# Kernel optimization log

Measured on AMD Instinct MI355X. Metric: run time of the kernel, lower is better.

## Reference

```python
import jax, jax.numpy as jnp
import numpy as np

H = 64          # hidden_size
FF = 36         # MLP hidden
B, W, S = 512, 8, 200


def setup_inputs() -> dict:
    key = jax.random.key(0)
    ks = jax.random.split(key, 8)
    query = jax.random.normal(ks[0], (B, H), dtype=jnp.float32)
    k = jax.random.normal(ks[1], (B, W, S, H), dtype=jnp.float32)
    mask = jax.random.randint(ks[2], (B, W, S, 1), 0, 2).astype(bool)
    # MLP params: Linear(4H -> 36), PReLU(scalar), Linear(36 -> 1)
    lim1 = 1.0 / np.sqrt(4 * H)
    W1 = jax.random.uniform(ks[3], (FF, 4 * H), jnp.float32, -lim1, lim1)
    b1 = jax.random.uniform(ks[4], (FF,), jnp.float32, -lim1, lim1)
    prelu_a = jnp.float32(0.25)
    lim2 = 1.0 / np.sqrt(FF)
    W2 = jax.random.uniform(ks[5], (1, FF), jnp.float32, -lim2, lim2)
    b2 = jax.random.uniform(ks[6], (1,), jnp.float32, -lim2, lim2)
    return {"query": query, "key": k, "W1": W1, "b1": b1,
            "prelu_a": prelu_a, "W2": W2, "b2": b2, "mask": mask}


def reference(query, key, W1, b1, prelu_a, W2, b2, mask):
    # broadcast query to (B, W, S, H)
    q = jnp.broadcast_to(query[:, None, None, :], key.shape)
    feat = jnp.concatenate([q, key, q - key, q * key], axis=-1)  # (B,W,S,4H)
    h = jnp.einsum('bwsf,of->bwso', feat, W1) + b1               # (B,W,S,36)
    h = jnp.where(h >= 0, h, prelu_a * h)                        # PReLU
    score = jnp.einsum('bwso,uo->bwsu', h, W2) + b2              # (B,W,S,1)
    # weighted_att=True: mask with -1e4 then softmax over seq_len
    score = jnp.where(mask, jnp.float32(-10000.0), score)
    score = jax.nn.softmax(score, axis=2)
    out = (key * score).sum(axis=2)                              # (B,W,H)
    return out
```

## Files before the change

### kernel.cpp

```cpp
#include <hip/hip_runtime.h>
#include <hip/hip_bf16.h>
#include <math.h>


#define BB   512
#define WW   8
#define SS   200
#define HH   64
#define FFN  36

typedef __attribute__((ext_vector_type(8))) short short8;
typedef __attribute__((ext_vector_type(4))) float f32x4;

__device__ __forceinline__ unsigned short f2bf(float x) {
    __hip_bfloat16 h = __float2bfloat16(x);
    union { __hip_bfloat16 b; unsigned short u; } c; c.b = h;
    return c.u;
}
__device__ __forceinline__ float bf2f(unsigned short h) {
    union { unsigned u; float f; } v; v.u = ((unsigned)h) << 16;
    return v.f;
}

__global__ __launch_bounds__(256)
void precompute_c(const float* __restrict__ query,
                  const float* __restrict__ W1,
                  const float* __restrict__ b1,
                  unsigned short* __restrict__ c_hi_g,
                  float* __restrict__ A_g)
{
    __shared__ float q_s[HH];
    const int b = blockIdx.x, tid = threadIdx.x;
    if (tid < HH) q_s[tid] = query[b * HH + tid];
    __syncthreads();
    for (int idx = tid; idx < 48 * HH; idx += 256) {
        int o = idx >> 6, h = idx & 63;
        float c = 0.0f;
        if (o < FFN) {
            const float* w = W1 + o * 4 * HH;
            c = w[HH + h] - w[2 * HH + h] + w[3 * HH + h] * q_s[h];
        }
        c_hi_g[(size_t)b * 48 * HH + idx] = f2bf(c);
    }
    if (tid < 48) {
        float a = 0.0f;
        if (tid < FFN) {
            const float* w = W1 + tid * 4 * HH;
            a = b1[tid];
            #pragma unroll 8
            for (int h = 0; h < HH; ++h) a += (w[h] + w[2 * HH + h]) * q_s[h];
        }
        A_g[b * 48 + tid] = a;
    }
}

__device__ __forceinline__ void load_tile(const float* __restrict__ kg,
                                          int st, int n, int q,
                                          float4 (&buf)[2][2])
{
    const int s = st * 16 + n;
    const float* p = kg + (size_t)s * HH + q * 8;
    if (s < SS) {
        buf[0][0] = *(const float4*)(p);
        buf[0][1] = *(const float4*)(p + 4);
        buf[1][0] = *(const float4*)(p + 32);
        buf[1][1] = *(const float4*)(p + 36);
    } else {
        const float4 z = make_float4(0.f, 0.f, 0.f, 0.f);
        buf[0][0] = z; buf[0][1] = z; buf[1][0] = z; buf[1][1] = z;
    }
}

__device__ __forceinline__ void compute_tile(const float4 (&buf)[2][2],
                                             const short8 (&Bf)[3][2],
                                             const float (&Ao)[3],
                                             const float (&w2o)[3],
                                             float pa, int st, int q, int n,
                                             float* __restrict__ scw)
{
    short8 Ah[2], Al[2];
    #pragma unroll
    for (int ks = 0; ks < 2; ++ks) {
        const float vv[8] = {buf[ks][0].x, buf[ks][0].y, buf[ks][0].z, buf[ks][0].w,
                             buf[ks][1].x, buf[ks][1].y, buf[ks][1].z, buf[ks][1].w};
        #pragma unroll
        for (int j = 0; j < 8; ++j) {
            const unsigned short hi = f2bf(vv[j]);
            Ah[ks][j] = (short)hi;
            Al[ks][j] = (short)f2bf(vv[j] - bf2f(hi));
        }
    }
    float contrib[4] = {0.f, 0.f, 0.f, 0.f};
    #pragma unroll
    for (int ot = 0; ot < 3; ++ot) {
        f32x4 acc = {0.f, 0.f, 0.f, 0.f};
        acc = __builtin_amdgcn_mfma_f32_16x16x32_bf16(Ah[0], Bf[ot][0], acc, 0, 0, 0);
        acc = __builtin_amdgcn_mfma_f32_16x16x32_bf16(Al[0], Bf[ot][0], acc, 0, 0, 0);
        acc = __builtin_amdgcn_mfma_f32_16x16x32_bf16(Ah[1], Bf[ot][1], acc, 0, 0, 0);
        acc = __builtin_amdgcn_mfma_f32_16x16x32_bf16(Al[1], Bf[ot][1], acc, 0, 0, 0);
        #pragma unroll
        for (int r = 0; r < 4; ++r) {
            float hv = acc[r] + Ao[ot];
            hv = (hv >= 0.0f) ? hv : pa * hv;
            contrib[r] += w2o[ot] * hv;
        }
    }
    #pragma unroll
    for (int m = 1; m <= 8; m <<= 1)
        #pragma unroll
        for (int r = 0; r < 4; ++r)
            contrib[r] += __shfl_xor(contrib[r], m, 64);
    if (n == 0) {
        #pragma unroll
        for (int r = 0; r < 4; ++r)
            scw[st * 16 + q * 4 + r] = contrib[r];
    }
}

__global__ __launch_bounds__(256, 4)
void twb_wave(const float* __restrict__ key,
              const unsigned short* __restrict__ c_hi_g,
              const float* __restrict__ A_g,
              const float* __restrict__ prelu_a,
              const float* __restrict__ W2,
              const int*   __restrict__ mask,
              float*       __restrict__ out)
{
    __shared__ float sc_s[4][208];

    const int tid  = threadIdx.x;
    const int wid  = tid >> 6, lane = tid & 63;
    const int q    = lane >> 4, n = lane & 15;
    const int bw   = blockIdx.x * 4 + wid;
    const int b    = bw >> 3;
    const float* kg = key + (size_t)bw * (SS * HH);
    float* scw = sc_s[wid];

    const unsigned short* cb = c_hi_g + (size_t)b * 48 * HH;
    short8 Bf[3][2];
    float  Ao[3], w2o[3];
    #pragma unroll
    for (int ot = 0; ot < 3; ++ot) {
        const int o = ot * 16 + n;
        #pragma unroll
        for (int ks = 0; ks < 2; ++ks)
            Bf[ot][ks] = *(const short8*)(cb + (size_t)o * HH + ks * 32 + q * 8);
        Ao[ot]  = A_g[b * 48 + o];
        w2o[ot] = (o < FFN) ? W2[o] : 0.0f;
    }
    const float pa = prelu_a[0];
    const int mv0 = mask[bw * SS + lane];
    const int mv1 = mask[bw * SS + 64 + lane];
    const int mv2 = mask[bw * SS + 128 + lane];
    const int mv3 = (lane < 8) ? mask[bw * SS + 192 + lane] : 1;

    float4 bufA[2][2], bufB[2][2];
    load_tile(kg, 0, n, q, bufA);
    for (int st2 = 0; st2 < 6; ++st2) {
        const int st = st2 * 2;
        load_tile(kg, st + 1, n, q, bufB);
        compute_tile(bufA, Bf, Ao, w2o, pa, st, q, n, scw);
        load_tile(kg, st + 2, n, q, bufA);
        compute_tile(bufB, Bf, Ao, w2o, pa, st + 1, q, n, scw);
    }
    compute_tile(bufA, Bf, Ao, w2o, pa, 12, q, n, scw);

    float sv0 = mv0 ? -10000.0f : scw[lane];
    float sv1 = mv1 ? -10000.0f : scw[64 + lane];
    float sv2 = mv2 ? -10000.0f : scw[128 + lane];
    float sv3 = (lane < 8) ? (mv3 ? -10000.0f : scw[192 + lane]) : -3.0e38f;
    float mx = fmaxf(fmaxf(sv0, sv1), fmaxf(sv2, sv3));
    #pragma unroll
    for (int off = 32; off > 0; off >>= 1)
        mx = fmaxf(mx, __shfl_xor(mx, off, 64));
    const float e0 = __expf(sv0 - mx);
    const float e1 = __expf(sv1 - mx);
    const float e2 = __expf(sv2 - mx);
    const float e3 = (lane < 8) ? __expf(sv3 - mx) : 0.0f;
    float ssum = e0 + e1 + e2 + e3;
    #pragma unroll
    for (int off = 32; off > 0; off >>= 1)
        ssum += __shfl_xor(ssum, off, 64);
    const float inv = 1.0f / ssum;
    scw[lane]       = e0 * inv;
    scw[64 + lane]  = e1 * inv;
    scw[128 + lane] = e2 * inv;
    if (lane < 8) scw[192 + lane] = e3 * inv;

    const int h4 = n * 4;
    float4 acc2 = make_float4(0.f, 0.f, 0.f, 0.f);
    #pragma unroll 5
    for (int s = q; s < SS; s += 4) {
        const float w = scw[s];
        const float4 kv = *(const float4*)(kg + (size_t)s * HH + h4);
        acc2.x += w * kv.x; acc2.y += w * kv.y;
        acc2.z += w * kv.z; acc2.w += w * kv.w;
    }
    #pragma unroll
    for (int off = 16; off <= 32; off <<= 1) {
        acc2.x += __shfl_xor(acc2.x, off, 64);
        acc2.y += __shfl_xor(acc2.y, off, 64);
        acc2.z += __shfl_xor(acc2.z, off, 64);
        acc2.w += __shfl_xor(acc2.w, off, 64);
    }
    if (lane < 16)
        *(float4*)(out + (size_t)bw * HH + h4) = acc2;
}

#define PADQ 17
__global__ __launch_bounds__(256, 2)
void twb_fallback(const float* __restrict__ query,
                  const float* __restrict__ key,
                  const float* __restrict__ W1,
                  const float* __restrict__ b1,
                  const float* __restrict__ prelu_a,
                  const float* __restrict__ W2,
                  const float* __restrict__ b2,
                  const int*   __restrict__ mask,
                  float*       __restrict__ out)
{
    __shared__ float q_s[HH];
    __shared__ float c_s[FFN * HH];
    __shared__ float A_s[FFN];
    __shared__ float W2_s[FFN];
    __shared__ float k_s[SS * PADQ * 4];
    __shared__ float wl[256];
    __shared__ float red[8];
    __shared__ float part[4 * 64];

    const int tid = threadIdx.x;
    const int bw  = blockIdx.x;
    const int b   = bw >> 3;

    if (tid < HH)  q_s[tid]  = query[b * HH + tid];
    if (tid < FFN) W2_s[tid] = W2[tid];
    __syncthreads();

    const float4* gk4 = (const float4*)(key + (size_t)bw * (SS * HH));
    float4* kl4 = (float4*)k_s;
    for (int i = tid; i < (SS * HH) / 4; i += 256) {
        float4 v = gk4[i];
        kl4[(i >> 4) * PADQ + (i & 15)] = v;
    }
    for (int idx = tid; idx < FFN * HH; idx += 256) {
        int o = idx >> 6, h = idx & 63;
        const float* w = W1 + o * (4 * HH);
        c_s[idx] = w[HH + h] - w[2 * HH + h] + w[3 * HH + h] * q_s[h];
    }
    if (tid < FFN) {
        const float* w = W1 + tid * (4 * HH);
        float a = b1[tid];
        for (int h = 0; h < HH; ++h) a += (w[h] + w[2 * HH + h]) * q_s[h];
        A_s[tid] = a;
    }
    __syncthreads();

    const float pa  = prelu_a[0];
    const float bb2 = b2[0];
    float msc = -3.0e38f;
    if (tid < SS) {
        float acc[FFN];
        #pragma unroll
        for (int o = 0; o < FFN; ++o) acc[o] = A_s[o];
        const float4* c4 = (const float4*)c_s;
        const float4* k4 = (const float4*)k_s;
        const int rowbase = tid * PADQ;
        for (int ch = 0; ch < 4; ++ch) {
            float4 kv0 = k4[rowbase + ch * 4 + 0];
            float4 kv1 = k4[rowbase + ch * 4 + 1];
            float4 kv2 = k4[rowbase + ch * 4 + 2];
            float4 kv3 = k4[rowbase + ch * 4 + 3];
            #pragma unroll
            for (int o = 0; o < FFN; ++o) {
                float4 c0 = c4[o * 16 + ch * 4 + 0];
                float4 c1 = c4[o * 16 + ch * 4 + 1];
                float4 c2 = c4[o * 16 + ch * 4 + 2];
                float4 c3 = c4[o * 16 + ch * 4 + 3];
                float a = acc[o];
                a += c0.x * kv0.x + c0.y * kv0.y + c0.z * kv0.z + c0.w * kv0.w;
                a += c1.x * kv1.x + c1.y * kv1.y + c1.z * kv1.z + c1.w * kv1.w;
                a += c2.x * kv2.x + c2.y * kv2.y + c2.z * kv2.z + c2.w * kv2.w;
                a += c3.x * kv3.x + c3.y * kv3.y + c3.z * kv3.z + c3.w * kv3.w;
                acc[o] = a;
            }
        }
        float sc = bb2;
        #pragma unroll
        for (int o = 0; o < FFN; ++o) {
            float a = acc[o];
            a = (a >= 0.0f) ? a : pa * a;
            sc += W2_s[o] * a;
        }
        msc = mask[bw * SS + tid] ? -10000.0f : sc;
    }

    float mx = msc;
    #pragma unroll
    for (int off = 32; off > 0; off >>= 1)
        mx = fmaxf(mx, __shfl_xor(mx, off, 64));
    const int wid = tid >> 6;
    if ((tid & 63) == 0) red[wid] = mx;
    __syncthreads();
    const float M = fmaxf(fmaxf(red[0], red[1]), fmaxf(red[2], red[3]));
    float e = (tid < SS) ? __expf(msc - M) : 0.0f;
    float ssum = e;
    #pragma unroll
    for (int off = 32; off > 0; off >>= 1)
        ssum += __shfl_xor(ssum, off, 64);
    if ((tid & 63) == 0) red[4 + wid] = ssum;
    __syncthreads();
    const float total = red[4] + red[5] + red[6] + red[7];
    if (tid < SS) wl[tid] = e / total;
    __syncthreads();

    const int wv = tid >> 6, h = tid & 63;
    float p = 0.0f;
    for (int s = wv * 50; s < wv * 50 + 50; ++s)
        p += k_s[s * (PADQ * 4) + h] * wl[s];
    part[wv * 64 + h] = p;
    __syncthreads();
    if (tid < 64) {
        float r = part[tid] + part[64 + tid] + part[128 + tid] + part[192 + tid];
        out[(size_t)bw * HH + tid] = r;
    }
}

extern "C" void kernel_launch(void* const* d_in, const int* in_sizes, int n_in,
                              void* d_out, int out_size, void* d_ws, size_t ws_size,
                              hipStream_t stream) {
    const float* query   = (const float*)d_in[0];
    const float* key     = (const float*)d_in[1];
    const float* W1      = (const float*)d_in[2];
    const float* b1      = (const float*)d_in[3];
    const float* prelu_a = (const float*)d_in[4];
    const float* W2      = (const float*)d_in[5];
    const float* b2      = (const float*)d_in[6];
    const int*   mask    = (const int*)d_in[7];
    float* out = (float*)d_out;

    const size_t c_bytes = (size_t)BB * 48 * HH * sizeof(unsigned short);
    const size_t a_bytes = (size_t)BB * 48 * sizeof(float);
    if (ws_size >= c_bytes + a_bytes) {
        unsigned short* c_hi_g = (unsigned short*)d_ws;
        float* A_g = (float*)((char*)d_ws + c_bytes);
        precompute_c<<<BB, 256, 0, stream>>>(query, W1, b1, c_hi_g, A_g);
        twb_wave<<<(BB * WW) / 4, 256, 0, stream>>>(key, c_hi_g, A_g, prelu_a,
                                                    W2, mask, out);
    } else {
        twb_fallback<<<BB * WW, 256, 0, stream>>>(query, key, W1, b1, prelu_a,
                                                  W2, b2, mask, out);
    }
}
```

Before: 322.7 us.

## Fuse softmax and weighted sum into a single online-softmax pass over key tiles

Replaces the three-phase scheme (score tiles into LDS, softmax, then a second read of key for the weighted sum) with a flash-style online softmax. Each tile's scores are redistributed to their rows, and a running max, running sum and 16 output accumulators per lane are rescaled and updated from key data already held in registers. This removes the second global read of key (about 420 MB) and the shared-memory score buffer. In exchange it adds per-tile shuffle reductions, extra exp calls and 16 more live registers per lane.

Measured after the change: 316.1 us. 2.0% less time.

```diff
diff --git a/kernel.cpp b/kernel.cpp
--- a/kernel.cpp
+++ b/kernel.cpp
@@ -71,12 +71,13 @@
     }
 }
 
-__device__ __forceinline__ void compute_tile(const float4 (&buf)[2][2],
-                                             const short8 (&Bf)[3][2],
-                                             const float (&Ao)[3],
-                                             const float (&w2o)[3],
-                                             float pa, int st, int q, int n,
-                                             float* __restrict__ scw)
+__device__ __forceinline__ void online_tile(const float4 (&buf)[2][2],
+                                            const short8 (&Bf)[3][2],
+                                            const float (&Ao)[3],
+                                            const float (&w2o)[3],
+                                            float pa, int st, int q, int n,
+                                            unsigned mbits,
+                                            float& m, float& l, float (&o)[16])
 {
     short8 Ah[2], Al[2];
     #pragma unroll
@@ -106,35 +107,64 @@
         }
     }
     #pragma unroll
-    for (int m = 1; m <= 8; m <<= 1)
+    for (int mm = 1; mm <= 8; mm <<= 1)
         #pragma unroll
         for (int r = 0; r < 4; ++r)
-            contrib[r] += __shfl_xor(contrib[r], m, 64);
-    if (n == 0) {
-        #pragma unroll
-        for (int r = 0; r < 4; ++r)
-            scw[st * 16 + q * 4 + r] = contrib[r];
+            contrib[r] += __shfl_xor(contrib[r], mm, 64);
+
+    const int rsel = n & 3;
+    float v = contrib[0];
+    v = (rsel == 1) ? contrib[1] : v;
+    v = (rsel == 2) ? contrib[2] : v;
+    v = (rsel == 3) ? contrib[3] : v;
+    const float srow = __shfl(v, ((n >> 2) << 4) | (n & 3), 64);
+
+    const int s_row = st * 16 + n;
+    float sn = (s_row < SS)
+             ? (((mbits >> st) & 1u) ? -10000.0f : srow)
+             : -3.0e38f;
+
+    float tm = sn;
+    #pragma unroll
+    for (int mm = 1; mm <= 8; mm <<= 1)
+        tm = fmaxf(tm, __shfl_xor(tm, mm, 64));
+    const float m_new = fmaxf(m, tm);
+    const float scl = __expf(m - m_new);
+    const float w   = __expf(sn - m_new);
+    float ls = w;
+    #pragma unroll
+    for (int mm = 1; mm <= 8; mm <<= 1)
+        ls += __shfl_xor(ls, mm, 64);
+    l = l * scl + ls;
+    m = m_new;
+    #pragma unroll
+    for (int ks = 0; ks < 2; ++ks) {
+        o[ks*8+0] = o[ks*8+0]*scl + w*buf[ks][0].x;
+        o[ks*8+1] = o[ks*8+1]*scl + w*buf[ks][0].y;
+        o[ks*8+2] = o[ks*8+2]*scl + w*buf[ks][0].z;
+        o[ks*8+3] = o[ks*8+3]*scl + w*buf[ks][0].w;
+        o[ks*8+4] = o[ks*8+4]*scl + w*buf[ks][1].x;
+        o[ks*8+5] = o[ks*8+5]*scl + w*buf[ks][1].y;
+        o[ks*8+6] = o[ks*8+6]*scl + w*buf[ks][1].z;
+        o[ks*8+7] = o[ks*8+7]*scl + w*buf[ks][1].w;
     }
 }
 
 __global__ __launch_bounds__(256, 4)
-void twb_wave(const float* __restrict__ key,
-              const unsigned short* __restrict__ c_hi_g,
-              const float* __restrict__ A_g,
-              const float* __restrict__ prelu_a,
-              const float* __restrict__ W2,
-              const int*   __restrict__ mask,
-              float*       __restrict__ out)
-{
-    __shared__ float sc_s[4][208];
-
+void twb_flash(const float* __restrict__ key,
+               const unsigned short* __restrict__ c_hi_g,
+               const float* __restrict__ A_g,
+               const float* __restrict__ prelu_a,
+               const float* __restrict__ W2,
+               const int*   __restrict__ mask,
+               float*       __restrict__ out)
+{
     const int tid  = threadIdx.x;
     const int wid  = tid >> 6, lane = tid & 63;
     const int q    = lane >> 4, n = lane & 15;
     const int bw   = blockIdx.x * 4 + wid;
     const int b    = bw >> 3;
     const float* kg = key + (size_t)bw * (SS * HH);
-    float* scw = sc_s[wid];
 
     const unsigned short* cb = c_hi_g + (size_t)b * 48 * HH;
     short8 Bf[3][2];
@@ -149,62 +179,49 @@
         w2o[ot] = (o < FFN) ? W2[o] : 0.0f;
     }
     const float pa = prelu_a[0];
-    const int mv0 = mask[bw * SS + lane];
-    const int mv1 = mask[bw * SS + 64 + lane];
-    const int mv2 = mask[bw * SS + 128 + lane];
-    const int mv3 = (lane < 8) ? mask[bw * SS + 192 + lane] : 1;
+
+    unsigned mbits = 0;
+    #pragma unroll
+    for (int st = 0; st < 13; ++st) {
+        const int s = st * 16 + n;
+        int mv = 1;
+        if (s < SS) mv = mask[bw * SS + s];
+        mbits |= (mv ? 1u : 0u) << st;
+    }
+
+    float m = -3.0e38f, l = 0.0f;
+    float o[16];
+    #pragma unroll
+    for (int j = 0; j < 16; ++j) o[j] = 0.0f;
 
     float4 bufA[2][2], bufB[2][2];
     load_tile(kg, 0, n, q, bufA);
     for (int st2 = 0; st2 < 6; ++st2) {
-        const int st = st2 * 2;
-        load_tile(kg, st + 1, n, q, bufB);
-        compute_tile(bufA, Bf, Ao, w2o, pa, st, q, n, scw);
-        load_tile(kg, st + 2, n, q, bufA);
-        compute_tile(bufB, Bf, Ao, w2o, pa, st + 1, q, n, scw);
-    }
-    compute_tile(bufA, Bf, Ao, w2o, pa, 12, q, n, scw);
-
-    float sv0 = mv0 ? -10000.0f : scw[lane];
-    float sv1 = mv1 ? -10000.0f : scw[64 + lane];
-    float sv2 = mv2 ? -10000.0f : scw[128 + lane];
-    float sv3 = (lane < 8) ? (mv3 ? -10000.0f : scw[192 + lane]) : -3.0e38f;
-    float mx = fmaxf(fmaxf(sv0, sv1), fmaxf(sv2, sv3));
-    #pragma unroll
-    for (int off = 32; off > 0; off >>= 1)
-        mx = fmaxf(mx, __shfl_xor(mx, off, 64));
-    const float e0 = __expf(sv0 - mx);
-    const float e1 = __expf(sv1 - mx);
-    const float e2 = __expf(sv2 - mx);
-    const float e3 = (lane < 8) ? __expf(sv3 - mx) : 0.0f;
-    float ssum = e0 + e1 + e2 + e3;
-    #pragma unroll
-    for (int off = 32; off > 0; off >>= 1)
-        ssum += __shfl_xor(ssum, off, 64);
-    const float inv = 1.0f / ssum;
-    scw[lane]       = e0 * inv;
-    scw[64 + lane]  = e1 * inv;
-    scw[128 + lane] = e2 * inv;
-    if (lane < 8) scw[192 + lane] = e3 * inv;
-
-    const int h4 = n * 4;
-    float4 acc2 = make_float4(0.f, 0.f, 0.f, 0.f);
-    #pragma unroll 5
-    for (int s = q; s < SS; s += 4) {
-        const float w = scw[s];
-        const float4 kv = *(const float4*)(kg + (size_t)s * HH + h4);
-        acc2.x += w * kv.x; acc2.y += w * kv.y;
-        acc2.z += w * kv.z; acc2.w += w * kv.w;
-    }
-    #pragma unroll
-    for (int off = 16; off <= 32; off <<= 1) {
-        acc2.x += __shfl_xor(acc2.x, off, 64);
-        acc2.y += __shfl_xor(acc2.y, off, 64);
-        acc2.z += __shfl_xor(acc2.z, off, 64);
-        acc2.w += __shfl_xor(acc2.w, off, 64);
-    }
-    if (lane < 16)
-        *(float4*)(out + (size_t)bw * HH + h4) = acc2;
+        load_tile(kg, st2 * 2 + 1, n, q, bufB);
+        online_tile(bufA, Bf, Ao, w2o, pa, st2 * 2, q, n, mbits, m, l, o);
+        load_tile(kg, st2 * 2 + 2, n, q, bufA);
+        online_tile(bufB, Bf, Ao, w2o, pa, st2 * 2 + 1, q, n, mbits, m, l, o);
+    }
+    online_tile(bufA, Bf, Ao, w2o, pa, 12, q, n, mbits, m, l, o);
+
+    #pragma unroll
+    for (int mm = 1; mm <= 8; mm <<= 1)
+        #pragma unroll
+        for (int j = 0; j < 16; ++j)
+            o[j] += __shfl_xor(o[j], mm, 64);
+    if (n == 0) {
+        const float inv = 1.0f / l;
+        float* po = out + (size_t)bw * HH;
+        float4 v;
+        v = make_float4(o[0]*inv,  o[1]*inv,  o[2]*inv,  o[3]*inv);
+        *(float4*)(po + q * 8)      = v;
+        v = make_float4(o[4]*inv,  o[5]*inv,  o[6]*inv,  o[7]*inv);
+        *(float4*)(po + q * 8 + 4)  = v;
+        v = make_float4(o[8]*inv,  o[9]*inv,  o[10]*inv, o[11]*inv);
+        *(float4*)(po + 32 + q * 8) = v;
+        v = make_float4(o[12]*inv, o[13]*inv, o[14]*inv, o[15]*inv);
+        *(float4*)(po + 36 + q * 8) = v;
+    }
 }
 
 #define PADQ 17
@@ -344,8 +361,8 @@
         unsigned short* c_hi_g = (unsigned short*)d_ws;
         float* A_g = (float*)((char*)d_ws + c_bytes);
         precompute_c<<<BB, 256, 0, stream>>>(query, W1, b1, c_hi_g, A_g);
-        twb_wave<<<(BB * WW) / 4, 256, 0, stream>>>(key, c_hi_g, A_g, prelu_a,
-                                                    W2, mask, out);
+        twb_flash<<<(BB * WW) / 4, 256, 0, stream>>>(key, c_hi_g, A_g, prelu_a,
+                                                     W2, mask, out);
     } else {
         twb_fallback<<<BB * WW, 256, 0, stream>>>(query, key, W1, b1, prelu_a,
                                                   W2, b2, mask, out);
```
